# Kernel tuning notes

Hardware: AMD Instinct MI355X
Metric: run time of the kernel (lower is better)

## Reference

```python
import jax, jax.numpy as jnp
import numpy as np

B, N0 = 16384, 2048
NUM_CLASSES, NUM_CLUSTERS, NDIM = 12, 24, 4
W_SCALE = 0.02  # keep logits in a sane range for softmax


def setup_inputs() -> dict:
    key = jax.random.key(0)
    ks = jax.random.split(key, 7)
    return {
        "x": jax.random.normal(ks[0], (B, N0), dtype=jnp.float32),
        "W_fc": jax.random.normal(ks[1], (N0, NUM_CLASSES), dtype=jnp.float32) * W_SCALE,
        "b_fc": jax.random.normal(ks[2], (NUM_CLASSES,), dtype=jnp.float32) * W_SCALE,
        "W_bin": jax.random.normal(ks[3], (NUM_CLASSES, N0, NUM_CLUSTERS), dtype=jnp.float32) * W_SCALE,
        "b_bin": jax.random.normal(ks[4], (NUM_CLASSES, NUM_CLUSTERS), dtype=jnp.float32) * W_SCALE,
        "W_res": jax.random.normal(ks[5], (NUM_CLASSES, N0, NDIM), dtype=jnp.float32) * W_SCALE,
        "b_res": jax.random.normal(ks[6], (NUM_CLASSES, NDIM), dtype=jnp.float32) * W_SCALE,
    }


def reference(x, W_fc, b_fc, W_bin, b_bin, W_res, b_res):
    # x: [B, N0] pre-extracted features (feature_model output)
    bsz = x.shape[0]
    C = W_bin.shape[0]

    # category head
    y0 = x @ W_fc + b_fc                                   # [B, C]
    Pc = jax.nn.softmax(y0, axis=1)                        # [B, C]

    # grouped per-class bin linears as one batched GEMM -> [B, K, C]
    y1 = jnp.einsum('bd,cdk->bkc', x, W_bin) + b_bin.T[None]
    Pl = jax.nn.softmax(y1, axis=1)                        # softmax over clusters
    Plc = Pl * Pc[:, None, :]                              # [B, K, C]

    # joint argmax over (cluster, class); torch flatten of [B,K,C] -> ic = ind % C
    ind = jnp.argmax(Plc.reshape(bsz, -1), axis=1)
    ic = ind % C                                           # selected class per row

    # direct gather replaces one-hot scatter + bmm
    y1_sel = jnp.take_along_axis(y1, ic[:, None, None], axis=2)[..., 0]   # [B, K]

    # grouped per-class residual linears -> [B, ndim, C], then gather
    y2 = jnp.einsum('bd,cdn->bnc', x, W_res) + b_res.T[None]
    y2_sel = jnp.take_along_axis(y2, ic[:, None, None], axis=2)[..., 0]   # [B, ndim]

    return (y0, y1_sel, y2_sel, Plc)
```

## Files before the change

kernel.cpp:

```cpp
#include <hip/hip_runtime.h>
#include <math.h>

#define BROWS 16384
#define N0    2048
#define NCLS  12
#define NCLU  24
#define NDIM  4
#define NCOL  348
#define NPAD  384
#define NTILE 24

#define OUT0_OFF 0
#define OUT1_OFF (BROWS * NCLS)
#define OUT2_OFF (OUT1_OFF + BROWS * NCLU)
#define OUT3_OFF (OUT2_OFF + BROWS * NDIM)

typedef __attribute__((ext_vector_type(8))) short bf16x8;
typedef __attribute__((ext_vector_type(4))) float f32x4;
typedef unsigned short ushort_t;

__device__ __forceinline__ unsigned short f2bf(float f) {
    unsigned u = __float_as_uint(f);
    u += 0x7fffu + ((u >> 16) & 1u);
    return (unsigned short)(u >> 16);
}
__device__ __forceinline__ float bf2f(unsigned short h) {
    return __uint_as_float(((unsigned)h) << 16);
}

__device__ __forceinline__ void cvt8pk(float4 a, float4 b, bf16x8& h, bf16x8& l) {
    unsigned h0, h1, h2, h3;
    asm("v_cvt_pk_bf16_f32 %0, %1, %2" : "=v"(h0) : "v"(a.x), "v"(a.y));
    asm("v_cvt_pk_bf16_f32 %0, %1, %2" : "=v"(h1) : "v"(a.z), "v"(a.w));
    asm("v_cvt_pk_bf16_f32 %0, %1, %2" : "=v"(h2) : "v"(b.x), "v"(b.y));
    asm("v_cvt_pk_bf16_f32 %0, %1, %2" : "=v"(h3) : "v"(b.z), "v"(b.w));
    float r0 = a.x - __uint_as_float(h0 << 16);
    float r1 = a.y - __uint_as_float(h0 & 0xffff0000u);
    float r2 = a.z - __uint_as_float(h1 << 16);
    float r3 = a.w - __uint_as_float(h1 & 0xffff0000u);
    float r4 = b.x - __uint_as_float(h2 << 16);
    float r5 = b.y - __uint_as_float(h2 & 0xffff0000u);
    float r6 = b.z - __uint_as_float(h3 << 16);
    float r7 = b.w - __uint_as_float(h3 & 0xffff0000u);
    unsigned l0, l1, l2, l3;
    asm("v_cvt_pk_bf16_f32 %0, %1, %2" : "=v"(l0) : "v"(r0), "v"(r1));
    asm("v_cvt_pk_bf16_f32 %0, %1, %2" : "=v"(l1) : "v"(r2), "v"(r3));
    asm("v_cvt_pk_bf16_f32 %0, %1, %2" : "=v"(l2) : "v"(r4), "v"(r5));
    asm("v_cvt_pk_bf16_f32 %0, %1, %2" : "=v"(l3) : "v"(r6), "v"(r7));
    union Pack { unsigned u[4]; bf16x8 v; };
    Pack H; H.u[0] = h0; H.u[1] = h1; H.u[2] = h2; H.u[3] = h3;
    Pack L; L.u[0] = l0; L.u[1] = l1; L.u[2] = l2; L.u[3] = l3;
    h = H.v;
    l = L.v;
}

__device__ __forceinline__ void load_lds16(const void* g, void* l) {
    __builtin_amdgcn_global_load_lds((const __attribute__((address_space(1))) void*)g,
                                     (__attribute__((address_space(3))) void*)l, 16, 0, 0);
}

__device__ __forceinline__ float fused_w(const float* __restrict__ W_fc,
                                         const float* __restrict__ W_bin,
                                         const float* __restrict__ W_res,
                                         int col, int d) {
    float w = 0.0f;
    if (col < NCLS) {
        w = W_fc[d * NCLS + col];
    } else if (col < 12 + NCLU * NCLS) {
        int jj = col - 12;
        int k = jj / NCLS, c = jj - k * NCLS;
        w = W_bin[((size_t)c * N0 + d) * NCLU + k];
    } else if (col < NCOL) {
        int jj = col - 300;
        int n = jj / NCLS, c = jj - n * NCLS;
        w = W_res[((size_t)c * N0 + d) * NDIM + n];
    }
    return w;
}

__global__ void jcp_repack3(const float* __restrict__ W_fc, const float* __restrict__ b_fc,
                            const float* __restrict__ W_bin, const float* __restrict__ b_bin,
                            const float* __restrict__ W_res, const float* __restrict__ b_res,
                            ushort_t* __restrict__ Bph, ushort_t* __restrict__ Bpl,
                            float* __restrict__ bias) {
    int t = blockIdx.x * 256 + threadIdx.x;
    if (t >= NTILE * 64 * 64) return;
    const int lane = t & 63;
    const int kb   = (t >> 6) & 63;
    const int J    = t >> 12;
    const int col  = J * 16 + (lane & 15);
    const int k0   = kb * 32 + (lane >> 4) * 8;

    bf16x8 h, l;
    #pragma unroll
    for (int i = 0; i < 8; ++i) {
        float w = fused_w(W_fc, W_bin, W_res, col, k0 + i);
        unsigned short hi = f2bf(w);
        h[i] = (short)hi;
        l[i] = (short)f2bf(w - bf2f(hi));
    }
    *(bf16x8*)(Bph + (size_t)t * 8) = h;
    *(bf16x8*)(Bpl + (size_t)t * 8) = l;

    if (t < NPAD) {
        int jb = t;
        float bv = 0.0f;
        if (jb < NCLS) {
            bv = b_fc[jb];
        } else if (jb < 12 + NCLU * NCLS) {
            int jj = jb - 12;
            int k = jj / NCLS, c = jj - k * NCLS;
            bv = b_bin[c * NCLU + k];
        } else if (jb < NCOL) {
            int jj = jb - 300;
            int n = jj / NCLS, c = jj - n * NCLS;
            bv = b_res[c * NDIM + n];
        }
        bias[jb] = bv;
    }
}

#define GBODY(CUR, NXT, PBUF, RBUF, IT)                                        \
    {                                                                          \
        _Pragma("unroll")                                                      \
        for (int j = 0; j < 3; ++j) {                                          \
            bh[NXT][j] = *(const bf16x8*)(pBh + Jt3[j] + ((IT) + 1) * 512);    \
            bl[NXT][j] = *(const bf16x8*)(pBl + Jt3[j] + ((IT) + 1) * 512);    \
        }                                                                      \
        __builtin_amdgcn_sched_barrier(0);                                     \
        _Pragma("unroll")                                                      \
        for (int n = 0; n < 4; ++n)                                            \
            load_lds16(gx + n * 65536 + ((IT) + 2) * 32,                       \
                       &Lx[(PBUF) * 4096 + n * 1024 + tid * 4]);               \
        __builtin_amdgcn_sched_barrier(0);                                     \
        __builtin_amdgcn_s_setprio(1);                                         \
        _Pragma("unroll")                                                      \
        for (int j = 0; j < 3; ++j) {                                          \
            _Pragma("unroll")                                                  \
            for (int rt = 0; rt < 4; ++rt) {                                   \
                acc[rt][j] = __builtin_amdgcn_mfma_f32_16x16x32_bf16(          \
                    Ah[CUR][rt], bh[CUR][j], acc[rt][j], 0, 0, 0);             \
                acc[rt][j] = __builtin_amdgcn_mfma_f32_16x16x32_bf16(          \
                    Al[CUR][rt], bh[CUR][j], acc[rt][j], 0, 0, 0);             \
                acc[rt][j] = __builtin_amdgcn_mfma_f32_16x16x32_bf16(          \
                    Ah[CUR][rt], bl[CUR][j], acc[rt][j], 0, 0, 0);             \
            }                                                                  \
        }                                                                      \
        __builtin_amdgcn_s_setprio(0);                                         \
        asm volatile("s_waitcnt vmcnt(10)" ::: "memory");                      \
        asm volatile("s_barrier" ::: "memory");                                \
        __builtin_amdgcn_sched_barrier(0);                                     \
        {                                                                      \
            const float* lx = &Lx[(RBUF) * 4096];                              \
            _Pragma("unroll")                                                  \
            for (int rt = 0; rt < 4; ++rt) {                                   \
                const int ro = (rg * 64 + rt * 16 + l16) * 32;                 \
                fa4[rt] = *(const float4*)&lx[ro + o1];                        \
                fb4[rt] = *(const float4*)&lx[ro + o2];                        \
            }                                                                  \
            asm volatile("s_waitcnt lgkmcnt(0)" ::: "memory");                 \
            __builtin_amdgcn_sched_barrier(0);                                 \
            _Pragma("unroll")                                                  \
            for (int rt = 0; rt < 4; ++rt)                                     \
                cvt8pk(fa4[rt], fb4[rt], Ah[NXT][rt], Al[NXT][rt]);            \
        }                                                                      \
        asm volatile("s_waitcnt vmcnt(4)" ::: "memory");                       \
        __builtin_amdgcn_sched_barrier(0);                                     \
        asm volatile("s_barrier" ::: "memory");                                \
    }

__global__ __launch_bounds__(256, 2) void jcp_gemm12(const float* __restrict__ x,
                                                     const ushort_t* __restrict__ Bph,
                                                     const ushort_t* __restrict__ Bpl,
                                                     const float* __restrict__ bias,
                                                     float* __restrict__ Y) {
    __shared__ float Lx[2 * 4096];

    const int tid  = threadIdx.x;
    const int wid  = tid >> 6;
    const int lane = tid & 63;
    const int quad = lane >> 4;
    const int l16  = lane & 15;
    const int rg   = wid & 1;
    const int cg   = wid >> 1;

    const int g   = blockIdx.x;
    const int xcd = g & 7;
    const int jj  = g >> 3;
    const int by  = xcd * 16 + (jj >> 2);
    const int bx  = jj & 3;
    const int rbase = by * 128;
    const int jbase = bx * 96;

    const int r0 = tid >> 3;
    const int c0 = tid & 7;
    const int o0 = c0 ^ (r0 & 7);
    const float* gx = x + (size_t)(rbase + r0) * N0 + o0 * 4;

    const ushort_t* pBh = Bph + (size_t)lane * 8;
    const ushort_t* pBl = Bpl + (size_t)lane * 8;
    int Jt3[3];
    #pragma unroll
    for (int j = 0; j < 3; ++j) Jt3[j] = (bx * 6 + cg * 3 + j) * 32768;

    const int s  = l16 & 7;
    const int o1 = ((2 * quad) ^ s) * 4;
    const int o2 = o1 ^ 4;

    f32x4 acc[4][3];
    #pragma unroll
    for (int rt = 0; rt < 4; ++rt)
        #pragma unroll
        for (int j = 0; j < 3; ++j)
            acc[rt][j] = f32x4{0.f, 0.f, 0.f, 0.f};

    bf16x8 Ah[2][4], Al[2][4], bh[2][3], bl[2][3];
    float4 fa4[4], fb4[4];

    #pragma unroll
    for (int n = 0; n < 4; ++n) load_lds16(gx + n * 65536, &Lx[n * 1024 + tid * 4]);
    __builtin_amdgcn_sched_barrier(0);
    #pragma unroll
    for (int j = 0; j < 3; ++j) {
        bh[0][j] = *(const bf16x8*)(pBh + Jt3[j]);
        bl[0][j] = *(const bf16x8*)(pBl + Jt3[j]);
    }
    __builtin_amdgcn_sched_barrier(0);
    #pragma unroll
    for (int n = 0; n < 4; ++n) load_lds16(gx + n * 65536 + 32, &Lx[4096 + n * 1024 + tid * 4]);
    __builtin_amdgcn_sched_barrier(0);
    asm volatile("s_waitcnt vmcnt(10)" ::: "memory");
    asm volatile("s_barrier" ::: "memory");
    __builtin_amdgcn_sched_barrier(0);
    {
        const float* lx = &Lx[0];
        #pragma unroll
        for (int rt = 0; rt < 4; ++rt) {
            const int ro = (rg * 64 + rt * 16 + l16) * 32;
            fa4[rt] = *(const float4*)&lx[ro + o1];
            fb4[rt] = *(const float4*)&lx[ro + o2];
        }
        asm volatile("s_waitcnt lgkmcnt(0)" ::: "memory");
        __builtin_amdgcn_sched_barrier(0);
        #pragma unroll
        for (int rt = 0; rt < 4; ++rt) cvt8pk(fa4[rt], fb4[rt], Ah[0][rt], Al[0][rt]);
    }
    asm volatile("s_waitcnt vmcnt(4)" ::: "memory");
    __builtin_amdgcn_sched_barrier(0);
    asm volatile("s_barrier" ::: "memory");

    for (int it = 0; it < 62; it += 2) {
        GBODY(0, 1, 0, 1, it);
        GBODY(1, 0, 1, 0, it + 1);
    }

    {
        #pragma unroll
        for (int j = 0; j < 3; ++j) {
            bh[1][j] = *(const bf16x8*)(pBh + Jt3[j] + 63 * 512);
            bl[1][j] = *(const bf16x8*)(pBl + Jt3[j] + 63 * 512);
        }
        __builtin_amdgcn_sched_barrier(0);
        __builtin_amdgcn_s_setprio(1);
        #pragma unroll
        for (int j = 0; j < 3; ++j)
            #pragma unroll
            for (int rt = 0; rt < 4; ++rt) {
                acc[rt][j] = __builtin_amdgcn_mfma_f32_16x16x32_bf16(Ah[0][rt], bh[0][j], acc[rt][j], 0, 0, 0);
                acc[rt][j] = __builtin_amdgcn_mfma_f32_16x16x32_bf16(Al[0][rt], bh[0][j], acc[rt][j], 0, 0, 0);
                acc[rt][j] = __builtin_amdgcn_mfma_f32_16x16x32_bf16(Ah[0][rt], bl[0][j], acc[rt][j], 0, 0, 0);
            }
        __builtin_amdgcn_s_setprio(0);
        asm volatile("s_waitcnt vmcnt(6)" ::: "memory");
        asm volatile("s_barrier" ::: "memory");
        __builtin_amdgcn_sched_barrier(0);
        const float* lx = &Lx[4096];
        #pragma unroll
        for (int rt = 0; rt < 4; ++rt) {
            const int ro = (rg * 64 + rt * 16 + l16) * 32;
            fa4[rt] = *(const float4*)&lx[ro + o1];
            fb4[rt] = *(const float4*)&lx[ro + o2];
        }
        asm volatile("s_waitcnt lgkmcnt(0)" ::: "memory");
        __builtin_amdgcn_sched_barrier(0);
        #pragma unroll
        for (int rt = 0; rt < 4; ++rt) cvt8pk(fa4[rt], fb4[rt], Ah[1][rt], Al[1][rt]);
        asm volatile("s_waitcnt vmcnt(0)" ::: "memory");
        __builtin_amdgcn_sched_barrier(0);
        #pragma unroll
        for (int j = 0; j < 3; ++j)
            #pragma unroll
            for (int rt = 0; rt < 4; ++rt) {
                acc[rt][j] = __builtin_amdgcn_mfma_f32_16x16x32_bf16(Ah[1][rt], bh[1][j], acc[rt][j], 0, 0, 0);
                acc[rt][j] = __builtin_amdgcn_mfma_f32_16x16x32_bf16(Al[1][rt], bh[1][j], acc[rt][j], 0, 0, 0);
                acc[rt][j] = __builtin_amdgcn_mfma_f32_16x16x32_bf16(Ah[1][rt], bl[1][j], acc[rt][j], 0, 0, 0);
            }
    }

    #pragma unroll
    for (int j = 0; j < 3; ++j) {
        const int col = jbase + cg * 48 + 16 * j + l16;
        const float bj = bias[col];
        #pragma unroll
        for (int rt = 0; rt < 4; ++rt) {
            float* yp = Y + (size_t)(rbase + rg * 64 + rt * 16 + quad * 4) * NPAD + col;
            yp[0 * NPAD] = acc[rt][j][0] + bj;
            yp[1 * NPAD] = acc[rt][j][1] + bj;
            yp[2 * NPAD] = acc[rt][j][2] + bj;
            yp[3 * NPAD] = acc[rt][j][3] + bj;
        }
    }
}

#define LROW 388

__global__ __launch_bounds__(256) void jcp_head4(const float* __restrict__ Y,
                                                 float* __restrict__ out) {
    __shared__ float Ly[16 * LROW];
    const int tid = threadIdx.x;
    const int r0  = blockIdx.x * 16;

    #pragma unroll
    for (int jj = 0; jj < 6; ++jj) {
        int f = tid + jj * 256;
        int row = f / 96, c4 = f - row * 96;
        float4 v = *(const float4*)(Y + (size_t)(r0 + row) * NPAD + c4 * 4);
        *(float4*)&Ly[row * LROW + c4 * 4] = v;
    }
    __syncthreads();

    const int grp = tid >> 4;
    const int c   = tid & 15;
    const bool on = (c < NCLS);
    const int r   = r0 + grp;
    const float* y = &Ly[grp * LROW];

    float y0c = on ? y[c] : -INFINITY;
    float m0 = y0c;
    #pragma unroll
    for (int m = 8; m >= 1; m >>= 1) m0 = fmaxf(m0, __shfl_xor(m0, m, 16));
    float e0 = on ? expf(y0c - m0) : 0.0f;
    float s0 = e0;
    #pragma unroll
    for (int m = 8; m >= 1; m >>= 1) s0 += __shfl_xor(s0, m, 16);
    const float Pc = e0 / s0;

    float v[NCLU];
    float mc = -INFINITY;
    #pragma unroll
    for (int k = 0; k < NCLU; ++k) {
        v[k] = y[12 + k * NCLS + c];
        mc = fmaxf(mc, v[k]);
    }
    float ev[NCLU];
    float sc = 0.0f;
    #pragma unroll
    for (int k = 0; k < NCLU; ++k) { ev[k] = expf(v[k] - mc); sc += ev[k]; }
    const float rs = Pc / sc;

    float y2c[NDIM];
    #pragma unroll
    for (int n = 0; n < NDIM; ++n) y2c[n] = y[300 + n * NCLS + c];

    float best = -INFINITY;
    int bk = 0;
    float* lrow = &Ly[grp * LROW];
    #pragma unroll
    for (int k = 0; k < NCLU; ++k) {
        const float p = ev[k] * rs;
        if (on) lrow[k * NCLS + c] = p;
        if (p > best) { best = p; bk = k; }
    }
    int flat = bk * NCLS + c;
    if (!on) { best = -INFINITY; flat = 1 << 30; }

    #pragma unroll
    for (int m = 8; m >= 1; m >>= 1) {
        const float op = __shfl_xor(best, m, 16);
        const int   of = __shfl_xor(flat, m, 16);
        if (op > best || (op == best && of < flat)) { best = op; flat = of; }
    }
    const int ic = flat % NCLS;

    if (on) out[OUT0_OFF + (size_t)r * NCLS + c] = y0c;
    if (c == ic) {
        float* o1v = out + OUT1_OFF + (size_t)r * NCLU;
        #pragma unroll
        for (int k = 0; k < NCLU; ++k) o1v[k] = v[k];
        float* o2v = out + OUT2_OFF + (size_t)r * NDIM;
        #pragma unroll
        for (int n = 0; n < NDIM; ++n) o2v[n] = y2c[n];
    }

    __syncthreads();
    #pragma unroll
    for (int jj = 0; jj < 5; ++jj) {
        int f = tid + jj * 256;
        if (f < 1152) {
            int row = f / 72, c4 = f - row * 72;
            *(float4*)(out + OUT3_OFF + (size_t)(r0 + row) * (NCLU * NCLS) + c4 * 4) =
                *(float4*)&Ly[row * LROW + c4 * 4];
        }
    }
}

extern "C" void kernel_launch(void* const* d_in, const int* in_sizes, int n_in,
                              void* d_out, int out_size, void* d_ws, size_t ws_size,
                              hipStream_t stream) {
    const float* x     = (const float*)d_in[0];
    const float* W_fc  = (const float*)d_in[1];
    const float* b_fc  = (const float*)d_in[2];
    const float* W_bin = (const float*)d_in[3];
    const float* b_bin = (const float*)d_in[4];
    const float* W_res = (const float*)d_in[5];
    const float* b_res = (const float*)d_in[6];
    float* out = (float*)d_out;

    ushort_t* Bph  = (ushort_t*)d_ws;
    ushort_t* Bpl  = Bph + NTILE * 64 * 64 * 8;
    float*    bias = (float*)(Bpl + NTILE * 64 * 64 * 8);
    float*    Yb   = bias + NPAD;

    jcp_repack3<<<384, 256, 0, stream>>>(W_fc, b_fc, W_bin, b_bin, W_res, b_res,
                                         Bph, Bpl, bias);
    jcp_gemm12<<<512, 256, 0, stream>>>(x, Bph, Bpl, bias, Yb);
    jcp_head4<<<BROWS / 16, 256, 0, stream>>>(Yb, out);
}
```

Before: 274.0 us.

## Split GEMM K dimension in two and sum partials in head kernel

The GEMM kernel now splits the 2048-wide reduction into two halves, which doubles the grid to 1024 blocks and raises the occupancy hint to 4 blocks per SM. Each half writes its own partial result buffer, with the bias added only in the first half. The head kernel reads both buffers and adds them. The aim is more parallelism and latency hiding, at the cost of an extra intermediate buffer write and read plus a larger workspace.

```diff
diff --git a/kernel.cpp b/kernel.cpp
--- a/kernel.cpp
+++ b/kernel.cpp
@@ -169,11 +169,12 @@
         asm volatile("s_barrier" ::: "memory");                                \
     }
 
-__global__ __launch_bounds__(256, 2) void jcp_gemm12(const float* __restrict__ x,
+__global__ __launch_bounds__(256, 4) void jcp_gemm13(const float* __restrict__ x,
                                                      const ushort_t* __restrict__ Bph,
                                                      const ushort_t* __restrict__ Bpl,
                                                      const float* __restrict__ bias,
-                                                     float* __restrict__ Y) {
+                                                     float* __restrict__ Y0,
+                                                     float* __restrict__ Y1) {
     __shared__ float Lx[2 * 4096];
 
     const int tid  = threadIdx.x;
@@ -187,18 +188,19 @@
     const int g   = blockIdx.x;
     const int xcd = g & 7;
     const int jj  = g >> 3;
-    const int by  = xcd * 16 + (jj >> 2);
-    const int bx  = jj & 3;
+    const int by  = xcd * 16 + (jj >> 3);
+    const int bx  = (jj >> 1) & 3;
+    const int ks  = jj & 1;
     const int rbase = by * 128;
     const int jbase = bx * 96;
 
     const int r0 = tid >> 3;
     const int c0 = tid & 7;
     const int o0 = c0 ^ (r0 & 7);
-    const float* gx = x + (size_t)(rbase + r0) * N0 + o0 * 4;
-
-    const ushort_t* pBh = Bph + (size_t)lane * 8;
-    const ushort_t* pBl = Bpl + (size_t)lane * 8;
+    const float* gx = x + (size_t)(rbase + r0) * N0 + ks * 1024 + o0 * 4;
+
+    const ushort_t* pBh = Bph + (size_t)lane * 8 + (size_t)ks * 32 * 512;
+    const ushort_t* pBl = Bpl + (size_t)lane * 8 + (size_t)ks * 32 * 512;
     int Jt3[3];
     #pragma unroll
     for (int j = 0; j < 3; ++j) Jt3[j] = (bx * 6 + cg * 3 + j) * 32768;
@@ -249,7 +251,7 @@
     __builtin_amdgcn_sched_barrier(0);
     asm volatile("s_barrier" ::: "memory");
 
-    for (int it = 0; it < 62; it += 2) {
+    for (int it = 0; it < 30; it += 2) {
         GBODY(0, 1, 0, 1, it);
         GBODY(1, 0, 1, 0, it + 1);
     }
@@ -257,8 +259,8 @@
     {
         #pragma unroll
         for (int j = 0; j < 3; ++j) {
-            bh[1][j] = *(const bf16x8*)(pBh + Jt3[j] + 63 * 512);
-            bl[1][j] = *(const bf16x8*)(pBl + Jt3[j] + 63 * 512);
+            bh[1][j] = *(const bf16x8*)(pBh + Jt3[j] + 31 * 512);
+            bl[1][j] = *(const bf16x8*)(pBl + Jt3[j] + 31 * 512);
         }
         __builtin_amdgcn_sched_barrier(0);
         __builtin_amdgcn_s_setprio(1);
@@ -297,13 +299,14 @@
             }
     }
 
+    float* Yp = ks ? Y1 : Y0;
     #pragma unroll
     for (int j = 0; j < 3; ++j) {
         const int col = jbase + cg * 48 + 16 * j + l16;
-        const float bj = bias[col];
+        const float bj = ks ? 0.0f : bias[col];
         #pragma unroll
         for (int rt = 0; rt < 4; ++rt) {
-            float* yp = Y + (size_t)(rbase + rg * 64 + rt * 16 + quad * 4) * NPAD + col;
+            float* yp = Yp + (size_t)(rbase + rg * 64 + rt * 16 + quad * 4) * NPAD + col;
             yp[0 * NPAD] = acc[rt][j][0] + bj;
             yp[1 * NPAD] = acc[rt][j][1] + bj;
             yp[2 * NPAD] = acc[rt][j][2] + bj;
@@ -314,7 +317,8 @@
 
 #define LROW 388
 
-__global__ __launch_bounds__(256) void jcp_head4(const float* __restrict__ Y,
+__global__ __launch_bounds__(256) void jcp_head5(const float* __restrict__ Y0,
+                                                 const float* __restrict__ Y1,
                                                  float* __restrict__ out) {
     __shared__ float Ly[16 * LROW];
     const int tid = threadIdx.x;
@@ -324,7 +328,9 @@
     for (int jj = 0; jj < 6; ++jj) {
         int f = tid + jj * 256;
         int row = f / 96, c4 = f - row * 96;
-        float4 v = *(const float4*)(Y + (size_t)(r0 + row) * NPAD + c4 * 4);
+        float4 a = *(const float4*)(Y0 + (size_t)(r0 + row) * NPAD + c4 * 4);
+        float4 b = *(const float4*)(Y1 + (size_t)(r0 + row) * NPAD + c4 * 4);
+        float4 v; v.x = a.x + b.x; v.y = a.y + b.y; v.z = a.z + b.z; v.w = a.w + b.w;
         *(float4*)&Ly[row * LROW + c4 * 4] = v;
     }
     __syncthreads();
@@ -419,10 +425,11 @@
     ushort_t* Bph  = (ushort_t*)d_ws;
     ushort_t* Bpl  = Bph + NTILE * 64 * 64 * 8;
     float*    bias = (float*)(Bpl + NTILE * 64 * 64 * 8);
-    float*    Yb   = bias + NPAD;
+    float*    Y0   = bias + NPAD;
+    float*    Y1   = Y0 + (size_t)BROWS * NPAD;
 
     jcp_repack3<<<384, 256, 0, stream>>>(W_fc, b_fc, W_bin, b_bin, W_res, b_res,
                                          Bph, Bpl, bias);
-    jcp_gemm12<<<512, 256, 0, stream>>>(x, Bph, Bpl, bias, Yb);
-    jcp_head4<<<BROWS / 16, 256, 0, stream>>>(Yb, out);
-}
+    jcp_gemm13<<<1024, 256, 0, stream>>>(x, Bph, Bpl, bias, Y0, Y1);
+    jcp_head5<<<BROWS / 16, 256, 0, stream>>>(Y0, Y1, out);
+}
```

After: 543.1 us. 1.98x slower.
